# Kernel tuning notes

Hardware: AMD Instinct MI355X
Metric: run time of the kernel (lower is better)

## Reference

```python
import jax, jax.numpy as jnp
import numpy as np

N, E, DIM, HID, LAYERS = 100000, 600000, 128, 256, 2
LN_EPS = 1e-5


def setup_inputs() -> dict:
    key = jax.random.key(0)
    ks = jax.random.split(key, 16)
    h = jax.random.normal(ks[0], (N, DIM), dtype=jnp.float32)
    edge_index = jax.random.randint(ks[1], (E, 2), 0, N, dtype=jnp.int64)
    edge_attr = jax.random.uniform(ks[2], (E, 1), dtype=jnp.float32)
    s = 0.02
    # edge MLP: Linear(2*DIM+1, HID) -> GELU -> Linear(HID, 1) -> Sigmoid
    edge_w1 = jax.random.normal(ks[3], (LAYERS, 2 * DIM + 1, HID), dtype=jnp.float32) * s
    edge_b1 = jnp.zeros((LAYERS, HID), dtype=jnp.float32)
    edge_w2 = jax.random.normal(ks[4], (LAYERS, HID, 1), dtype=jnp.float32) * s
    edge_b2 = jnp.zeros((LAYERS, 1), dtype=jnp.float32)
    # node MLP: Linear(2*DIM, HID) -> GELU -> Linear(HID, DIM)
    node_w1 = jax.random.normal(ks[5], (LAYERS, 2 * DIM, HID), dtype=jnp.float32) * s
    node_b1 = jnp.zeros((LAYERS, HID), dtype=jnp.float32)
    node_w2 = jax.random.normal(ks[6], (LAYERS, HID, DIM), dtype=jnp.float32) * s
    node_b2 = jnp.zeros((LAYERS, DIM), dtype=jnp.float32)
    ln_g = jnp.ones((LAYERS, DIM), dtype=jnp.float32)
    ln_b = jnp.zeros((LAYERS, DIM), dtype=jnp.float32)
    return {"h": h, "edge_index": edge_index, "edge_attr": edge_attr,
            "edge_w1": edge_w1, "edge_b1": edge_b1, "edge_w2": edge_w2, "edge_b2": edge_b2,
            "node_w1": node_w1, "node_b1": node_b1, "node_w2": node_w2, "node_b2": node_b2,
            "ln_g": ln_g, "ln_b": ln_b}


def _layernorm(x, g, b):
    mu = jnp.mean(x, axis=-1, keepdims=True)
    var = jnp.mean(jnp.square(x - mu), axis=-1, keepdims=True)
    return (x - mu) * jax.lax.rsqrt(var + LN_EPS) * g + b


def reference(h, edge_index, edge_attr, edge_w1, edge_b1, edge_w2, edge_b2,
              node_w1, node_b1, node_w2, node_b2, ln_g, ln_b):
    src = edge_index[:, 0]
    dst = edge_index[:, 1]
    n = h.shape[0]
    for i in range(LAYERS):
        h_src = h[src]                                  # [E, DIM]
        h_dst = h[dst]                                  # [E, DIM]
        x = jnp.concatenate([h_src, h_dst, edge_attr], axis=-1)  # [E, 2*DIM+1]
        g1 = jax.nn.gelu(x @ edge_w1[i] + edge_b1[i], approximate=False)
        gate = jax.nn.sigmoid(g1 @ edge_w2[i] + edge_b2[i])       # [E, 1]
        msg = h_src * gate                              # [E, DIM]
        agg = jax.ops.segment_sum(msg, dst, num_segments=n)       # [N, DIM]
        den = jax.ops.segment_sum(gate, dst, num_segments=n)      # [N, 1]
        agg = agg / jnp.maximum(den, 1e-6)
        u = jnp.concatenate([h, agg], axis=-1)          # [N, 2*DIM]
        upd = jax.nn.gelu(u @ node_w1[i] + node_b1[i], approximate=False) @ node_w2[i] + node_b2[i]
        h = _layernorm(h + upd, ln_g[i], ln_b[i])
    return h
```

## Files before the change

kernel.cpp:

```cpp
#include <hip/hip_runtime.h>
#include <math.h>

#define NNODE 100000
#define NEDGE 600000
#define DIM 128
#define HID 256
#define NLAYERS 2

typedef short bf16x8 __attribute__((ext_vector_type(8)));
typedef short bf16x4 __attribute__((ext_vector_type(4)));
typedef float f32x4 __attribute__((ext_vector_type(4)));
typedef float f32x2 __attribute__((ext_vector_type(2)));

#define WK 136
#define WLD 264
#define LUTN 2048

__device__ __forceinline__ short f2bf(float x) {
    union { float f; unsigned u; } v; v.f = x;
    unsigned r = v.u + 0x7FFFu + ((v.u >> 16) & 1u);
    return (short)(r >> 16);
}
__device__ __forceinline__ float bf2f(short s) {
    union { unsigned u; float f; } v; v.u = ((unsigned)(unsigned short)s) << 16;
    return v.f;
}
__device__ __forceinline__ float gelu_erf(float x) {
    float z = x * 0.70710678118654752f;
    float az = fabsf(z);
    float t = __builtin_amdgcn_rcpf(1.0f + 0.3275911f * az);
    float y = t * (0.254829592f + t * (-0.284496736f + t * (1.421413741f +
              t * (-1.453152027f + t * 1.061405429f))));
    float e = __expf(-az * az);
    float er = 1.0f - y * e;
    er = copysignf(er, z);
    return 0.5f * x * (1.0f + er);
}
__device__ __forceinline__ float lut_look(const float* __restrict__ lut, float x) {
    float t = fmaf(x, 128.f, 1024.5f);
    t = fminf(fmaxf(t, 0.f), 2047.f);
    return lut[(int)t];
}

__global__ void prep_weights(const float* __restrict__ ew1,
                             const float* __restrict__ eb1,
                             const float* __restrict__ ew2,
                             const float* __restrict__ nw1,
                             const float* __restrict__ nw2,
                             const float* __restrict__ h0,
                             const int* __restrict__ ei,
                             short* __restrict__ pW,
                             short* __restrict__ nW1T,
                             short* __restrict__ nW2T,
                             float* __restrict__ w1a_p,
                             float* __restrict__ b1_p,
                             float* __restrict__ w2_p,
                             short* __restrict__ hb,
                             unsigned char* __restrict__ h8,
                             float* __restrict__ luts,
                             int* __restrict__ deg)
{
    int idx = blockIdx.x * 256 + threadIdx.x;
    const int SZ1 = NLAYERS * 512 * 128;
    const int SZ2 = NLAYERS * 256 * 256;
    const int SZ3 = NLAYERS * 128 * 256;
    const int SZ4 = NLAYERS * 256;
    const int SZH = NNODE * DIM / 8;
    if (idx < SZ1) {
        int L = idx / (512 * 128); int rr = idx - L * 512 * 128;
        int r = rr >> 7, k = rr & 127;
        int srow = (r < 256) ? k : 128 + k;
        int scol = (r < 256) ? r : r - 256;
        pW[(size_t)L * 512 * WK + r * WK + k] = f2bf(ew1[(size_t)L * 257 * 256 + srow * 256 + scol]);
        return;
    }
    idx -= SZ1;
    if (idx < SZ2) {
        int L = idx >> 16, r = idx & 65535, n = r >> 8, k = r & 255;
        nW1T[(size_t)L * 256 * WLD + n * WLD + k] = f2bf(nw1[(size_t)L * 256 * 256 + k * 256 + n]);
        return;
    }
    idx -= SZ2;
    if (idx < SZ3) {
        int L = idx >> 15, r = idx & 32767, n = r >> 8, k = r & 255;
        nW2T[(size_t)L * 128 * WLD + n * WLD + k] = f2bf(nw2[(size_t)L * 256 * 128 + k * 128 + n]);
        return;
    }
    idx -= SZ3;
    if (idx < SZ4) {
        int L = idx >> 8, c = idx & 255;
        int cs = (c & ~63) | ((c & 3) * 16 + ((c >> 2) & 15));
        w1a_p[idx] = ew1[(size_t)L * 257 * 256 + 256 * 256 + cs];
        b1_p[idx]  = eb1[(size_t)L * 256 + cs];
        w2_p[idx]  = ew2[(size_t)L * 256 + cs];
        return;
    }
    idx -= SZ4;
    if (idx < SZH) {
        const float4* p = (const float4*)(h0 + (size_t)idx * 8);
        float4 a = p[0], b = p[1];
        bf16x8 t;
        t[0] = f2bf(a.x); t[1] = f2bf(a.y); t[2] = f2bf(a.z); t[3] = f2bf(a.w);
        t[4] = f2bf(b.x); t[5] = f2bf(b.y); t[6] = f2bf(b.z); t[7] = f2bf(b.w);
        *(bf16x8*)(hb + (size_t)idx * 8) = t;
        int wa = __builtin_amdgcn_cvt_pk_fp8_f32(a.x, a.y, 0, false);
        wa = __builtin_amdgcn_cvt_pk_fp8_f32(a.z, a.w, wa, true);
        int wb = __builtin_amdgcn_cvt_pk_fp8_f32(b.x, b.y, 0, false);
        wb = __builtin_amdgcn_cvt_pk_fp8_f32(b.z, b.w, wb, true);
        *(unsigned*)(h8 + (size_t)idx * 8) = (unsigned)wa;
        *(unsigned*)(h8 + (size_t)idx * 8 + 4) = (unsigned)wb;
        return;
    }
    idx -= SZH;
    if (idx < 2 * LUTN) {
        int i = idx & (LUTN - 1);
        float x = (float)(i - 1024) * (1.0f / 128.0f);
        float v;
        if (idx < LUTN) {
            v = 0.5f * x * (1.0f + erff(x * 0.70710678118654752f));
        } else {
            v = 1.0f / (1.0f + expf(-x));
        }
        luts[idx] = v;
        return;
    }
    idx -= 2 * LUTN;
    if (idx < NEDGE) {
        atomicAdd(&deg[ei[2 * idx + 1]], 1);
    }
}

__global__ __launch_bounds__(1024)
void csr_scan(const int* __restrict__ deg, int* __restrict__ rowptr, int* __restrict__ cursor) {
    __shared__ int wsum[16];
    __shared__ int carry_s;
    const int tid = threadIdx.x, lane = tid & 63, wv = tid >> 6;
    if (tid == 0) carry_s = 0;
    __syncthreads();
    for (int base = 0; base < NNODE; base += 4096) {
        int i0 = base + tid * 4;
        int v0 = 0, v1 = 0, v2 = 0, v3 = 0;
        if (i0 + 3 < NNODE) {
            int4 q = *(const int4*)(deg + i0);
            v0 = q.x; v1 = q.y; v2 = q.z; v3 = q.w;
        } else if (i0 < NNODE) {
            v0 = deg[i0];
            if (i0 + 1 < NNODE) v1 = deg[i0 + 1];
            if (i0 + 2 < NNODE) v2 = deg[i0 + 2];
        }
        int tsum = v0 + v1 + v2 + v3;
        int x = tsum;
#pragma unroll
        for (int off = 1; off < 64; off <<= 1) {
            int y = __shfl_up(x, off);
            if (lane >= off) x += y;
        }
        if (lane == 63) wsum[wv] = x;
        __syncthreads();
        if (wv == 0) {
            int s = (lane < 16) ? wsum[lane] : 0;
#pragma unroll
            for (int off = 1; off < 16; off <<= 1) {
                int y = __shfl_up(s, off);
                if (lane >= off) s += y;
            }
            if (lane < 16) wsum[lane] = s;
        }
        __syncthreads();
        int carry = carry_s;
        int woff = wv ? wsum[wv - 1] : 0;
        int e0 = carry + woff + (x - tsum);
        if (i0 < NNODE)     { rowptr[i0] = e0;                cursor[i0] = e0; }
        if (i0 + 1 < NNODE) { int v = e0 + v0;                rowptr[i0+1] = v; cursor[i0+1] = v; }
        if (i0 + 2 < NNODE) { int v = e0 + v0 + v1;           rowptr[i0+2] = v; cursor[i0+2] = v; }
        if (i0 + 3 < NNODE) { int v = e0 + v0 + v1 + v2;      rowptr[i0+3] = v; cursor[i0+3] = v; }
        int total = wsum[15];
        __syncthreads();
        if (tid == 0) carry_s = carry + total;
        __syncthreads();
    }
    if (tid == 0) rowptr[NNODE] = carry_s;
}

__global__ void csr_scatter(const int* __restrict__ ei, const float* __restrict__ attr,
                            int* __restrict__ cursor, int2* __restrict__ epk) {
    int e = blockIdx.x * 256 + threadIdx.x;
    if (e >= NEDGE) return;
    int s = ei[2 * e], d = ei[2 * e + 1];
    int pos = atomicAdd(&cursor[d], 1);
    int2 pk; pk.x = s; pk.y = __float_as_int(attr[e]);
    epk[pos] = pk;
    if (e == 0) { int2 z; z.x = 0; z.y = 0; epk[NEDGE] = z; }
}

__global__ __launch_bounds__(512, 2)
void proj_kernel(const short* __restrict__ hb,
                 const short* __restrict__ pW,
                 unsigned char* __restrict__ Ps8,
                 short* __restrict__ Pd)
{
    __shared__ short A[64][WK];
    const int tid = threadIdx.x;
    const int n0 = blockIdx.x * 64;

    for (int idx = tid; idx < 64 * 16; idx += 512) {
        int nl = idx >> 4, q = idx & 15;
        int gn = min(n0 + nl, NNODE - 1);
        *(bf16x8*)&A[nl][q * 8] = *(const bf16x8*)(hb + (size_t)gn * DIM + q * 8);
    }
    __syncthreads();

    const int lane = tid & 63;
    const int wv = tid >> 6;
    const int lrow = lane & 15;
    const int lkg = lane >> 4;

    f32x4 acc[4][4];
#pragma unroll
    for (int mi = 0; mi < 4; ++mi)
#pragma unroll
        for (int ni = 0; ni < 4; ++ni) acc[mi][ni] = (f32x4){0.f, 0.f, 0.f, 0.f};

    const short* xbase = &A[lrow][lkg * 8];
    const short* wbase = pW + (size_t)(wv * 64 + lrow) * WK + lkg * 8;

#pragma unroll
    for (int kt = 0; kt < 4; ++kt) {
        bf16x8 a[4], b[4];
#pragma unroll
        for (int mi = 0; mi < 4; ++mi)
            a[mi] = *(const bf16x8*)(xbase + mi * 16 * WK + kt * 32);
#pragma unroll
        for (int ni = 0; ni < 4; ++ni)
            b[ni] = *(const bf16x8*)(wbase + ni * 16 * WK + kt * 32);
#pragma unroll
        for (int mi = 0; mi < 4; ++mi)
#pragma unroll
            for (int ni = 0; ni < 4; ++ni)
                acc[mi][ni] = __builtin_amdgcn_mfma_f32_16x16x32_bf16(a[mi], b[ni], acc[mi][ni], 0, 0, 0);
    }

    const int cb = (wv & 3) * 64;
    if (wv < 4) {
#pragma unroll
        for (int mi = 0; mi < 4; ++mi)
#pragma unroll
            for (int reg = 0; reg < 4; ++reg) {
                int node = n0 + mi * 16 + lkg * 4 + reg;
                int w = __builtin_amdgcn_cvt_pk_fp8_f32(acc[mi][0][reg], acc[mi][1][reg], 0, false);
                w = __builtin_amdgcn_cvt_pk_fp8_f32(acc[mi][2][reg], acc[mi][3][reg], w, true);
                if (node < NNODE)
                    *(unsigned*)(Ps8 + (size_t)node * 256 + cb + lrow * 4) = (unsigned)w;
            }
    } else {
#pragma unroll
        for (int mi = 0; mi < 4; ++mi)
#pragma unroll
            for (int reg = 0; reg < 4; ++reg) {
                int node = n0 + mi * 16 + lkg * 4 + reg;
                bf16x4 t;
                t[0] = f2bf(acc[mi][0][reg]);
                t[1] = f2bf(acc[mi][1][reg]);
                t[2] = f2bf(acc[mi][2][reg]);
                t[3] = f2bf(acc[mi][3][reg]);
                if (node < NNODE)
                    *(bf16x4*)(Pd + (size_t)node * 256 + cb + lrow * 4) = t;
            }
    }
}

__global__ __launch_bounds__(256)
void edge_agg(const unsigned char* __restrict__ Ps8, const short* __restrict__ Pd,
              const unsigned char* __restrict__ h8,
              const int2* __restrict__ epk, const int* __restrict__ rowptr,
              const float* __restrict__ w1a_p, const float* __restrict__ b1_p,
              const float* __restrict__ w2_p, const float* __restrict__ b2,
              const float* __restrict__ luts,
              short* __restrict__ u2)
{
    __shared__ float sg[LUTN];
    __shared__ float ss[LUTN];

    const int tid = threadIdx.x;
#pragma unroll
    for (int i = 0; i < LUTN / 256; ++i) {
        sg[tid + i * 256] = luts[tid + i * 256];
        ss[tid + i * 256] = luts[LUTN + tid + i * 256];
    }
    __syncthreads();

    const int node = (blockIdx.x * 256 + tid) >> 6;
    const int lane = tid & 63;

    const int beg = __builtin_amdgcn_readfirstlane(rowptr[node]);
    const int end = __builtin_amdgcn_readfirstlane(rowptr[node + 1]);
    const int d = end - beg;

    const float4 w1av = ((const float4*)w1a_p)[lane];
    const float4 b1v  = ((const float4*)b1_p)[lane];
    const float4 w2v  = ((const float4*)w2_p)[lane];
    const float b2s = b2[0];

    bf16x4 pd = *(const bf16x4*)(Pd + (size_t)node * 256 + lane * 4);
    const float pb0 = bf2f(pd[0]) + b1v.x;
    const float pb1 = bf2f(pd[1]) + b1v.y;
    const float pb2 = bf2f(pd[2]) + b1v.z;
    const float pb3 = bf2f(pd[3]) + b1v.w;

    const int2* ep = epk + beg;
    const int pso = lane * 4;
    const int hvo = lane * 2;

    float ax = 0.f, ay = 0.f, den = 0.f;

    unsigned ps_n = 0;
    unsigned short hv_n = 0;
    float a_n = 0.f;
    if (d > 0) {
        int2 sa = ep[0];
        int s0 = __builtin_amdgcn_readfirstlane(sa.x);
        a_n = __int_as_float(__builtin_amdgcn_readfirstlane(sa.y));
        ps_n = *(const unsigned*)(Ps8 + ((size_t)s0 << 8) + pso);
        hv_n = *(const unsigned short*)(h8 + ((size_t)s0 << 7) + hvo);
    }
    for (int t = 0; t < d; ++t) {
        unsigned psu = ps_n; unsigned short hv = hv_n; float a = a_n;
        {
            int2 sa = ep[t + 1];
            int s2 = __builtin_amdgcn_readfirstlane(sa.x);
            a_n = __int_as_float(__builtin_amdgcn_readfirstlane(sa.y));
            ps_n = *(const unsigned*)(Ps8 + ((size_t)s2 << 8) + pso);
            hv_n = *(const unsigned short*)(h8 + ((size_t)s2 << 7) + hvo);
        }
        f32x2 plo = __builtin_amdgcn_cvt_pk_f32_fp8((int)psu, false);
        f32x2 phi = __builtin_amdgcn_cvt_pk_f32_fp8((int)psu, true);
        float x0 = plo[0] + pb0 + a * w1av.x;
        float x1 = plo[1] + pb1 + a * w1av.y;
        float x2 = phi[0] + pb2 + a * w1av.z;
        float x3 = phi[1] + pb3 + a * w1av.w;
        float p = lut_look(sg, x0) * w2v.x + lut_look(sg, x1) * w2v.y +
                  lut_look(sg, x2) * w2v.z + lut_look(sg, x3) * w2v.w;
        p += __shfl_xor(p, 1);
        p += __shfl_xor(p, 2);
        p += __shfl_xor(p, 4);
        p += __shfl_xor(p, 8);
        p += __shfl_xor(p, 16);
        p += __shfl_xor(p, 32);
        float g = lut_look(ss, p + b2s);
        f32x2 hxy = __builtin_amdgcn_cvt_pk_f32_fp8((int)(unsigned)hv, false);
        ax = fmaf(g, hxy[0], ax);
        ay = fmaf(g, hxy[1], ay);
        den += g;
    }

    float dd = fmaxf(den, 1e-6f);
    float dinv = __builtin_amdgcn_rcpf(dd);
    dinv = dinv * (2.0f - dd * dinv);
    unsigned pk = (((unsigned)(unsigned short)f2bf(ay * dinv)) << 16) |
                  (unsigned)(unsigned short)f2bf(ax * dinv);
    *(unsigned*)(u2 + (size_t)node * 256 + lane * 2) = pk;
}

__global__ __launch_bounds__(256, 4)
void node_mlp(const float* __restrict__ hin,
              const short* __restrict__ hb,
              const short* __restrict__ u2,
              const short* __restrict__ W1T,
              const float* __restrict__ b1,
              const short* __restrict__ W2T,
              const float* __restrict__ b2,
              const float* __restrict__ lng, const float* __restrict__ lnb,
              float* __restrict__ hout, short* __restrict__ hb_out,
              unsigned char* __restrict__ h8_out)
{
    __shared__ short U[64][WLD];

    const int tid = threadIdx.x;
    const int n0 = blockIdx.x * 64;
    const int lane = tid & 63;
    const int wv = tid >> 6;

    for (int idx = tid; idx < 64 * 32; idx += 256) {
        int nl = idx >> 5, q = idx & 31;
        int gn = min(n0 + nl, NNODE - 1);
        const short* src = (q < 16) ? (hb + (size_t)gn * DIM + q * 8)
                                    : (u2 + (size_t)gn * 256 + (q - 16) * 8);
        *(bf16x8*)&U[nl][q * 8] = *(const bf16x8*)src;
    }
    __syncthreads();

    const int lrow = lane & 15;
    const int lkg = lane >> 4;
    const int n0w = wv * 64;

    f32x4 acc1[4][4];
#pragma unroll
    for (int mi = 0; mi < 4; ++mi)
#pragma unroll
        for (int ni = 0; ni < 4; ++ni) acc1[mi][ni] = (f32x4){0.f, 0.f, 0.f, 0.f};
    {
        const short* xbase = &U[lrow][lkg * 8];
        const short* wbase = W1T + (size_t)(n0w + lrow) * WLD + lkg * 8;
#pragma unroll
        for (int kt = 0; kt < 8; ++kt) {
            bf16x8 a[4], b[4];
#pragma unroll
            for (int mi = 0; mi < 4; ++mi)
                a[mi] = *(const bf16x8*)(xbase + mi * 16 * WLD + kt * 32);
#pragma unroll
            for (int ni = 0; ni < 4; ++ni)
                b[ni] = *(const bf16x8*)(wbase + ni * 16 * WLD + kt * 32);
#pragma unroll
            for (int mi = 0; mi < 4; ++mi)
#pragma unroll
                for (int ni = 0; ni < 4; ++ni)
                    acc1[mi][ni] = __builtin_amdgcn_mfma_f32_16x16x32_bf16(a[mi], b[ni], acc1[mi][ni], 0, 0, 0);
        }
    }
    __syncthreads();

    {
        float b1v[4];
#pragma unroll
        for (int ni = 0; ni < 4; ++ni) b1v[ni] = b1[n0w + ni * 16 + lrow];
#pragma unroll
        for (int mi = 0; mi < 4; ++mi)
#pragma unroll
            for (int ni = 0; ni < 4; ++ni)
#pragma unroll
                for (int reg = 0; reg < 4; ++reg) {
                    int row = mi * 16 + lkg * 4 + reg;
                    int col = n0w + ni * 16 + lrow;
                    U[row][col] = f2bf(gelu_erf(acc1[mi][ni][reg] + b1v[ni]));
                }
    }
    __syncthreads();

    f32x4 acc2[4][2];
#pragma unroll
    for (int mi = 0; mi < 4; ++mi)
#pragma unroll
        for (int ni = 0; ni < 2; ++ni) acc2[mi][ni] = (f32x4){0.f, 0.f, 0.f, 0.f};
    {
        const short* xbase = &U[lrow][lkg * 8];
        const short* wbase = W2T + (size_t)(wv * 32 + lrow) * WLD + lkg * 8;
#pragma unroll
        for (int kt = 0; kt < 8; ++kt) {
            bf16x8 a[4], b[2];
#pragma unroll
            for (int mi = 0; mi < 4; ++mi)
                a[mi] = *(const bf16x8*)(xbase + mi * 16 * WLD + kt * 32);
#pragma unroll
            for (int ni = 0; ni < 2; ++ni)
                b[ni] = *(const bf16x8*)(wbase + ni * 16 * WLD + kt * 32);
#pragma unroll
            for (int mi = 0; mi < 4; ++mi)
#pragma unroll
                for (int ni = 0; ni < 2; ++ni)
                    acc2[mi][ni] = __builtin_amdgcn_mfma_f32_16x16x32_bf16(a[mi], b[ni], acc2[mi][ni], 0, 0, 0);
        }
    }
    __syncthreads();

    float* R = (float*)&U[0][0];
    {
        float b2v[2];
#pragma unroll
        for (int ni = 0; ni < 2; ++ni) b2v[ni] = b2[wv * 32 + ni * 16 + lrow];
#pragma unroll
        for (int mi = 0; mi < 4; ++mi)
#pragma unroll
            for (int ni = 0; ni < 2; ++ni)
#pragma unroll
                for (int reg = 0; reg < 4; ++reg) {
                    int row = mi * 16 + lkg * 4 + reg;
                    int col = wv * 32 + ni * 16 + lrow;
                    R[row * 132 + col] = acc2[mi][ni][reg] + b2v[ni];
                }
    }
    __syncthreads();

#pragma unroll
    for (int ii = 0; ii < 16; ++ii) {
        int nl = wv * 16 + ii;
        int gn = n0 + nl;
        int gnc = min(gn, NNODE - 1);
        float rx = R[nl * 132 + lane * 2 + 0];
        float ry = R[nl * 132 + lane * 2 + 1];
        const float2 hh = *(const float2*)(hin + (size_t)gnc * DIM + lane * 2);
        float vx = rx + hh.x, vy = ry + hh.y;
        float s = vx + vy;
#pragma unroll
        for (int off = 32; off > 0; off >>= 1) s += __shfl_xor(s, off);
        float mu = s * (1.0f / 128.0f);
        float dx = vx - mu, dy = vy - mu;
        float q = dx * dx + dy * dy;
#pragma unroll
        for (int off = 32; off > 0; off >>= 1) q += __shfl_xor(q, off);
        float inv = rsqrtf(q * (1.0f / 128.0f) + 1e-5f);
        if (gn < NNODE) {
            const float2 gg = *(const float2*)(lng + lane * 2);
            const float2 bb = *(const float2*)(lnb + lane * 2);
            float ox = dx * inv * gg.x + bb.x;
            float oy = dy * inv * gg.y + bb.y;
            *(float2*)(hout + (size_t)gn * DIM + lane * 2) = make_float2(ox, oy);
            unsigned pk = ((unsigned)(unsigned short)f2bf(oy) << 16) |
                          (unsigned)(unsigned short)f2bf(ox);
            *(unsigned*)(hb_out + (size_t)gn * DIM + lane * 2) = pk;
            int w8 = __builtin_amdgcn_cvt_pk_fp8_f32(ox, oy, 0, false);
            *(unsigned short*)(h8_out + (size_t)gn * DIM + lane * 2) = (unsigned short)(w8 & 0xFFFF);
        }
    }
}

extern "C" void kernel_launch(void* const* d_in, const int* in_sizes, int n_in,
                              void* d_out, int out_size, void* d_ws, size_t ws_size,
                              hipStream_t stream) {
    const float* h0   = (const float*)d_in[0];
    const int*   ei   = (const int*)d_in[1];
    const float* attr = (const float*)d_in[2];
    const float* ew1  = (const float*)d_in[3];
    const float* eb1  = (const float*)d_in[4];
    const float* ew2  = (const float*)d_in[5];
    const float* eb2  = (const float*)d_in[6];
    const float* nw1  = (const float*)d_in[7];
    const float* nb1  = (const float*)d_in[8];
    const float* nw2  = (const float*)d_in[9];
    const float* nb2  = (const float*)d_in[10];
    const float* lng  = (const float*)d_in[11];
    const float* lnb  = (const float*)d_in[12];

    float* hout = (float*)d_out;

    char* p = (char*)d_ws;
    int*   rowptr = (int*)p;               p += sizeof(int) * (NNODE + 4);
    int*   cursor = (int*)p;               p += sizeof(int) * (NNODE + 4);
    int*   deg    = (int*)p;               p += sizeof(int) * (NNODE + 4);
    int2*  epk    = (int2*)p;              p += sizeof(int2) * (NEDGE + 1);
    short* hb     = (short*)p;             p += sizeof(short) * (size_t)NNODE * DIM;
    unsigned char* h8 = (unsigned char*)p; p += (size_t)NNODE * DIM;
    unsigned char* Ps8 = (unsigned char*)p; p += (size_t)NNODE * 256;
    short* Pd     = (short*)p;             p += sizeof(short) * (size_t)NNODE * 256;
    short* u2     = Pd;
    short* pW     = (short*)p;             p += sizeof(short) * (size_t)NLAYERS * 512 * WK;
    short* nW1T   = (short*)p;             p += sizeof(short) * (size_t)NLAYERS * 256 * WLD;
    short* nW2T   = (short*)p;             p += sizeof(short) * (size_t)NLAYERS * 128 * WLD;
    float* w1a_p  = (float*)p;             p += sizeof(float) * NLAYERS * 256;
    float* b1_p   = (float*)p;             p += sizeof(float) * NLAYERS * 256;
    float* w2_p   = (float*)p;             p += sizeof(float) * NLAYERS * 256;
    float* luts   = (float*)p;             p += sizeof(float) * 2 * LUTN;

    const int PREP_TOTAL = NLAYERS * 512 * 128 + NLAYERS * 256 * 256 +
                           NLAYERS * 128 * 256 + NLAYERS * 256 + NNODE * DIM / 8 +
                           2 * LUTN + NEDGE;

    hipMemsetAsync(deg, 0, (NNODE + 1) * sizeof(int), stream);
    prep_weights<<<(PREP_TOTAL + 255) / 256, 256, 0, stream>>>(
        ew1, eb1, ew2, nw1, nw2, h0, ei, pW, nW1T, nW2T, w1a_p, b1_p, w2_p, hb, h8, luts, deg);
    csr_scan<<<1, 1024, 0, stream>>>(deg, rowptr, cursor);
    csr_scatter<<<(NEDGE + 255) / 256, 256, 0, stream>>>(ei, attr, cursor, epk);

    for (int L = 0; L < NLAYERS; ++L) {
        const float* hin = (L == 0) ? h0 : hout;
        proj_kernel<<<(NNODE + 63) / 64, 512, 0, stream>>>(
            hb, pW + (size_t)L * 512 * WK, Ps8, Pd);
        edge_agg<<<NNODE / 4, 256, 0, stream>>>(
            Ps8, Pd, h8, epk, rowptr,
            w1a_p + (size_t)L * 256, b1_p + (size_t)L * 256,
            w2_p + (size_t)L * 256, eb2 + L, luts, u2);
        node_mlp<<<(NNODE + 63) / 64, 256, 0, stream>>>(
            hin, hb, u2,
            nW1T + (size_t)L * 256 * WLD, nb1 + (size_t)L * 256,
            nW2T + (size_t)L * 128 * WLD, nb2 + (size_t)L * 128,
            lng + (size_t)L * DIM, lnb + (size_t)L * DIM,
            hout, hb, h8);
    }
}
```

Baseline: 495.8 us.

## Fold CSR scan into proj kernel, batch edge gathers, use sigmoid GELU

The single-block CSR scan now runs as an extra block of the first-layer projection kernel, so it overlaps with projection work and one serial launch goes away. The edge aggregation loop loads up to 64 edge records per wave at once and prefetches four gathers at a time instead of doing one serial readfirstlane load per edge. The node MLP replaces the erf-based GELU with a sigmoid approximation, x*sigmoid(1.702x), which is cheaper but less accurate. The approximation may change outputs beyond tolerance.

```diff
diff --git a/kernel.cpp b/kernel.cpp
--- a/kernel.cpp
+++ b/kernel.cpp
@@ -6,6 +6,7 @@
 #define DIM 128
 #define HID 256
 #define NLAYERS 2
+#define PROJ_BLOCKS 1563
 
 typedef short bf16x8 __attribute__((ext_vector_type(8)));
 typedef short bf16x4 __attribute__((ext_vector_type(4)));
@@ -25,16 +26,9 @@
     union { unsigned u; float f; } v; v.u = ((unsigned)(unsigned short)s) << 16;
     return v.f;
 }
-__device__ __forceinline__ float gelu_erf(float x) {
-    float z = x * 0.70710678118654752f;
-    float az = fabsf(z);
-    float t = __builtin_amdgcn_rcpf(1.0f + 0.3275911f * az);
-    float y = t * (0.254829592f + t * (-0.284496736f + t * (1.421413741f +
-              t * (-1.453152027f + t * 1.061405429f))));
-    float e = __expf(-az * az);
-    float er = 1.0f - y * e;
-    er = copysignf(er, z);
-    return 0.5f * x * (1.0f + er);
+__device__ __forceinline__ float gelu_fast(float x) {
+    float e = exp2f(-2.4554673f * x);
+    return x * __builtin_amdgcn_rcpf(1.0f + e);
 }
 __device__ __forceinline__ float lut_look(const float* __restrict__ lut, float x) {
     float t = fmaf(x, 128.f, 1024.5f);
@@ -130,14 +124,25 @@
     }
 }
 
-__global__ __launch_bounds__(1024)
-void csr_scan(const int* __restrict__ deg, int* __restrict__ rowptr, int* __restrict__ cursor) {
-    __shared__ int wsum[16];
+__global__ void csr_scatter(const int* __restrict__ ei, const float* __restrict__ attr,
+                            int* __restrict__ cursor, int2* __restrict__ epk) {
+    int e = blockIdx.x * 256 + threadIdx.x;
+    if (e >= NEDGE) return;
+    int s = ei[2 * e], d = ei[2 * e + 1];
+    int pos = atomicAdd(&cursor[d], 1);
+    int2 pk; pk.x = s; pk.y = __float_as_int(attr[e]);
+    epk[pos] = pk;
+    if (e == 0) { int2 z; z.x = 0; z.y = 0; epk[NEDGE] = z; }
+}
+
+__device__ void scan_block512(const int* __restrict__ deg, int* __restrict__ rowptr,
+                              int* __restrict__ cursor) {
+    __shared__ int wsum[8];
     __shared__ int carry_s;
     const int tid = threadIdx.x, lane = tid & 63, wv = tid >> 6;
     if (tid == 0) carry_s = 0;
     __syncthreads();
-    for (int base = 0; base < NNODE; base += 4096) {
+    for (int base = 0; base < NNODE; base += 2048) {
         int i0 = base + tid * 4;
         int v0 = 0, v1 = 0, v2 = 0, v3 = 0;
         if (i0 + 3 < NNODE) {
@@ -158,13 +163,13 @@
         if (lane == 63) wsum[wv] = x;
         __syncthreads();
         if (wv == 0) {
-            int s = (lane < 16) ? wsum[lane] : 0;
-#pragma unroll
-            for (int off = 1; off < 16; off <<= 1) {
+            int s = (lane < 8) ? wsum[lane] : 0;
+#pragma unroll
+            for (int off = 1; off < 8; off <<= 1) {
                 int y = __shfl_up(s, off);
                 if (lane >= off) s += y;
             }
-            if (lane < 16) wsum[lane] = s;
+            if (lane < 8) wsum[lane] = s;
         }
         __syncthreads();
         int carry = carry_s;
@@ -174,31 +179,27 @@
         if (i0 + 1 < NNODE) { int v = e0 + v0;                rowptr[i0+1] = v; cursor[i0+1] = v; }
         if (i0 + 2 < NNODE) { int v = e0 + v0 + v1;           rowptr[i0+2] = v; cursor[i0+2] = v; }
         if (i0 + 3 < NNODE) { int v = e0 + v0 + v1 + v2;      rowptr[i0+3] = v; cursor[i0+3] = v; }
-        int total = wsum[15];
+        int total = wsum[7];
         __syncthreads();
         if (tid == 0) carry_s = carry + total;
         __syncthreads();
     }
     if (tid == 0) rowptr[NNODE] = carry_s;
-}
-
-__global__ void csr_scatter(const int* __restrict__ ei, const float* __restrict__ attr,
-                            int* __restrict__ cursor, int2* __restrict__ epk) {
-    int e = blockIdx.x * 256 + threadIdx.x;
-    if (e >= NEDGE) return;
-    int s = ei[2 * e], d = ei[2 * e + 1];
-    int pos = atomicAdd(&cursor[d], 1);
-    int2 pk; pk.x = s; pk.y = __float_as_int(attr[e]);
-    epk[pos] = pk;
-    if (e == 0) { int2 z; z.x = 0; z.y = 0; epk[NEDGE] = z; }
 }
 
 __global__ __launch_bounds__(512, 2)
 void proj_kernel(const short* __restrict__ hb,
                  const short* __restrict__ pW,
                  unsigned char* __restrict__ Ps8,
-                 short* __restrict__ Pd)
+                 short* __restrict__ Pd,
+                 const int* __restrict__ deg, int* __restrict__ rowptr,
+                 int* __restrict__ cursor)
 {
+    if (blockIdx.x >= PROJ_BLOCKS) {
+        scan_block512(deg, rowptr, cursor);
+        return;
+    }
+
     __shared__ short A[64][WK];
     const int tid = threadIdx.x;
     const int n0 = blockIdx.x * 64;
@@ -307,50 +308,72 @@
     const float pb2 = bf2f(pd[2]) + b1v.z;
     const float pb3 = bf2f(pd[3]) + b1v.w;
 
-    const int2* ep = epk + beg;
-    const int pso = lane * 4;
-    const int hvo = lane * 2;
+    const unsigned pso = (unsigned)(lane * 4);
+    const unsigned hvo = (unsigned)(lane * 2);
 
     float ax = 0.f, ay = 0.f, den = 0.f;
 
-    unsigned ps_n = 0;
-    unsigned short hv_n = 0;
-    float a_n = 0.f;
     if (d > 0) {
-        int2 sa = ep[0];
-        int s0 = __builtin_amdgcn_readfirstlane(sa.x);
-        a_n = __int_as_float(__builtin_amdgcn_readfirstlane(sa.y));
-        ps_n = *(const unsigned*)(Ps8 + ((size_t)s0 << 8) + pso);
-        hv_n = *(const unsigned short*)(h8 + ((size_t)s0 << 7) + hvo);
-    }
-    for (int t = 0; t < d; ++t) {
-        unsigned psu = ps_n; unsigned short hv = hv_n; float a = a_n;
-        {
-            int2 sa = ep[t + 1];
-            int s2 = __builtin_amdgcn_readfirstlane(sa.x);
-            a_n = __int_as_float(__builtin_amdgcn_readfirstlane(sa.y));
-            ps_n = *(const unsigned*)(Ps8 + ((size_t)s2 << 8) + pso);
-            hv_n = *(const unsigned short*)(h8 + ((size_t)s2 << 7) + hvo);
-        }
-        f32x2 plo = __builtin_amdgcn_cvt_pk_f32_fp8((int)psu, false);
-        f32x2 phi = __builtin_amdgcn_cvt_pk_f32_fp8((int)psu, true);
-        float x0 = plo[0] + pb0 + a * w1av.x;
-        float x1 = plo[1] + pb1 + a * w1av.y;
-        float x2 = phi[0] + pb2 + a * w1av.z;
-        float x3 = phi[1] + pb3 + a * w1av.w;
-        float p = lut_look(sg, x0) * w2v.x + lut_look(sg, x1) * w2v.y +
-                  lut_look(sg, x2) * w2v.z + lut_look(sg, x3) * w2v.w;
-        p += __shfl_xor(p, 1);
-        p += __shfl_xor(p, 2);
-        p += __shfl_xor(p, 4);
-        p += __shfl_xor(p, 8);
-        p += __shfl_xor(p, 16);
-        p += __shfl_xor(p, 32);
-        float g = lut_look(ss, p + b2s);
-        f32x2 hxy = __builtin_amdgcn_cvt_pk_f32_fp8((int)(unsigned)hv, false);
-        ax = fmaf(g, hxy[0], ax);
-        ay = fmaf(g, hxy[1], ay);
-        den += g;
+        const int dm = min(d, 64);
+        const int dm1 = dm - 1;
+
+        int2 sa0 = epk[beg + min(lane, d - 1)];
+        int sl = sa0.x;
+        float al = __int_as_float(sa0.y);
+
+        auto gather = [&](int T, unsigned& PS, unsigned& HV) {
+            int s_ = __shfl(sl, min(T, dm1));
+            PS = *(const unsigned*)(Ps8 + (((unsigned)s_ << 8) + pso));
+            HV = (unsigned)*(const unsigned short*)(h8 + (((unsigned)s_ << 7) + hvo));
+        };
+        auto edge_one = [&](float a, unsigned PSU, unsigned HVU) {
+            f32x2 plo = __builtin_amdgcn_cvt_pk_f32_fp8((int)PSU, false);
+            f32x2 phi = __builtin_amdgcn_cvt_pk_f32_fp8((int)PSU, true);
+            float x0 = plo[0] + pb0 + a * w1av.x;
+            float x1 = plo[1] + pb1 + a * w1av.y;
+            float x2 = phi[0] + pb2 + a * w1av.z;
+            float x3 = phi[1] + pb3 + a * w1av.w;
+            float p = lut_look(sg, x0) * w2v.x + lut_look(sg, x1) * w2v.y +
+                      lut_look(sg, x2) * w2v.z + lut_look(sg, x3) * w2v.w;
+            p += __shfl_xor(p, 1);
+            p += __shfl_xor(p, 2);
+            p += __shfl_xor(p, 4);
+            p += __shfl_xor(p, 8);
+            p += __shfl_xor(p, 16);
+            p += __shfl_xor(p, 32);
+            float g = lut_look(ss, p + b2s);
+            f32x2 hxy = __builtin_amdgcn_cvt_pk_f32_fp8((int)HVU, false);
+            ax = fmaf(g, hxy[0], ax);
+            ay = fmaf(g, hxy[1], ay);
+            den += g;
+        };
+
+        unsigned pA0, pA1, pA2, pA3, hA0, hA1, hA2, hA3;
+        unsigned pB0, pB1, pB2, pB3, hB0, hB1, hB2, hB3;
+        gather(0, pA0, hA0); gather(1, pA1, hA1);
+        gather(2, pA2, hA2); gather(3, pA3, hA3);
+
+        for (int t = 0; t < dm; t += 4) {
+            gather(t + 4, pB0, hB0); gather(t + 5, pB1, hB1);
+            gather(t + 6, pB2, hB2); gather(t + 7, pB3, hB3);
+
+            edge_one(__shfl(al, t), pA0, hA0);
+            if (t + 1 < dm) edge_one(__shfl(al, t + 1), pA1, hA1);
+            if (t + 2 < dm) edge_one(__shfl(al, t + 2), pA2, hA2);
+            if (t + 3 < dm) edge_one(__shfl(al, t + 3), pA3, hA3);
+
+            pA0 = pB0; pA1 = pB1; pA2 = pB2; pA3 = pB3;
+            hA0 = hB0; hA1 = hB1; hA2 = hB2; hA3 = hB3;
+        }
+
+        for (int t2 = 64; t2 < d; ++t2) {
+            int2 sa = epk[beg + t2];
+            int s_ = __builtin_amdgcn_readfirstlane(sa.x);
+            float a = __int_as_float(__builtin_amdgcn_readfirstlane(sa.y));
+            unsigned PS = *(const unsigned*)(Ps8 + (((unsigned)s_ << 8) + pso));
+            unsigned HV = (unsigned)*(const unsigned short*)(h8 + (((unsigned)s_ << 7) + hvo));
+            edge_one(a, PS, HV);
+        }
     }
 
     float dd = fmaxf(den, 1e-6f);
@@ -431,7 +454,7 @@
                 for (int reg = 0; reg < 4; ++reg) {
                     int row = mi * 16 + lkg * 4 + reg;
                     int col = n0w + ni * 16 + lrow;
-                    U[row][col] = f2bf(gelu_erf(acc1[mi][ni][reg] + b1v[ni]));
+                    U[row][col] = f2bf(gelu_fast(acc1[mi][ni][reg] + b1v[ni]));
                 }
     }
     __syncthreads();
@@ -557,13 +580,13 @@
     hipMemsetAsync(deg, 0, (NNODE + 1) * sizeof(int), stream);
     prep_weights<<<(PREP_TOTAL + 255) / 256, 256, 0, stream>>>(
         ew1, eb1, ew2, nw1, nw2, h0, ei, pW, nW1T, nW2T, w1a_p, b1_p, w2_p, hb, h8, luts, deg);
-    csr_scan<<<1, 1024, 0, stream>>>(deg, rowptr, cursor);
-    csr_scatter<<<(NEDGE + 255) / 256, 256, 0, stream>>>(ei, attr, cursor, epk);
 
     for (int L = 0; L < NLAYERS; ++L) {
         const float* hin = (L == 0) ? h0 : hout;
-        proj_kernel<<<(NNODE + 63) / 64, 512, 0, stream>>>(
-            hb, pW + (size_t)L * 512 * WK, Ps8, Pd);
+        proj_kernel<<<PROJ_BLOCKS + (L == 0 ? 1 : 0), 512, 0, stream>>>(
+            hb, pW + (size_t)L * 512 * WK, Ps8, Pd, deg, rowptr, cursor);
+        if (L == 0)
+            csr_scatter<<<(NEDGE + 255) / 256, 256, 0, stream>>>(ei, attr, cursor, epk);
         edge_agg<<<NNODE / 4, 256, 0, stream>>>(
             Ps8, Pd, h8, epk, rowptr,
             w1a_p + (size_t)L * 256, b1_p + (size_t)L * 256,
```

Measured after the change: 523.7 us. 1.06x slower.
